# Optimization experiments

Measured on AMD Instinct MI355X. Metric: run time of the kernel, lower is better.

Reference implementation:

```python
import jax, jax.numpy as jnp
import numpy as np

NT, NRV, NR = 100000, 200000, 300000  # tile / road_vertex / road node counts
E = 400000                             # edges per edge type
B, H, P, A = 64, 128, 64, 512          # graphs, hidden, player_state_dim, action_dim


def _gat(h_src, h_dst, src, dst, W, a_s, a_d, b, n_dst):
    # PyG GATConv, heads=1, shared lin for src/dst, no self loops (bipartite)
    hs = h_src @ W                      # [Ns, H]
    hd = h_dst @ W                      # [Nd, H]
    e = jax.nn.leaky_relu((hs @ a_s)[src] + (hd @ a_d)[dst], 0.2)  # [E]
    m = jax.ops.segment_max(e, dst, num_segments=n_dst)
    w = jnp.exp(e - m[dst])
    denom = jax.ops.segment_sum(w, dst, num_segments=n_dst)
    alpha = w / jnp.maximum(denom[dst], 1e-16)                      # segment softmax
    out = jax.ops.segment_sum(alpha[:, None] * hs[src], dst, num_segments=n_dst)
    return out + b


def _mean_pool(x, batch, nb):
    s = jax.ops.segment_sum(x, batch, num_segments=nb)
    c = jax.ops.segment_sum(jnp.ones((x.shape[0],), x.dtype), batch, num_segments=nb)
    return s / jnp.maximum(c, 1.0)[:, None]


def setup_inputs():
    ks = iter(jax.random.split(jax.random.key(0), 64))
    f32 = jnp.float32

    def lin(i, o):
        return (jax.random.normal(next(ks), (i, o), f32) / np.float32(np.sqrt(i)))

    d = {}
    d['x_tile'] = jax.random.normal(next(ks), (NT, 8), f32)
    d['x_rv'] = jax.random.normal(next(ks), (NRV, 13), f32)
    d['x_road'] = jax.random.normal(next(ks), (NR, 4), f32)
    d['x_player'] = jax.random.normal(next(ks), (B, P), f32)
    # node encoders
    d['enc_t_W'] = lin(8, H);  d['enc_t_b'] = jnp.zeros((H,), f32)
    d['enc_rv_W'] = lin(13, H); d['enc_rv_b'] = jnp.zeros((H,), f32)
    d['enc_r_W'] = lin(4, H);  d['enc_r_b'] = jnp.zeros((H,), f32)
    # six GAT convs
    for name in ['rv2t', 't2rv', 'r2rv', 'rv2r', 't2r', 'r2t']:
        d[name + '_W'] = lin(H, H)
        d[name + '_as'] = jax.random.normal(next(ks), (H,), f32) * 0.1
        d[name + '_ad'] = jax.random.normal(next(ks), (H,), f32) * 0.1
        d[name + '_b'] = jnp.zeros((H,), f32)
    # player MLP + output head (input: 3H pooled + H player)
    d['fc1_W'] = lin(P, H); d['fc1_b'] = jnp.zeros((H,), f32)
    d['fc2_W'] = lin(H, H); d['fc2_b'] = jnp.zeros((H,), f32)
    d['out_W'] = lin(4 * H, A); d['out_b'] = jnp.zeros((A,), f32)
    # edges (src bounded by source-type count, dst by dest-type count)
    ri = lambda n, hi: jax.random.randint(n, (E,), 0, hi, jnp.int32)
    d['e_rv2t_src'] = ri(next(ks), NRV); d['e_rv2t_dst'] = ri(next(ks), NT)
    d['e_t2rv_src'] = ri(next(ks), NT);  d['e_t2rv_dst'] = ri(next(ks), NRV)
    d['e_r2rv_src'] = ri(next(ks), NR);  d['e_r2rv_dst'] = ri(next(ks), NRV)
    d['e_rv2r_src'] = ri(next(ks), NRV); d['e_rv2r_dst'] = ri(next(ks), NR)
    d['e_t2r_src'] = ri(next(ks), NT);   d['e_t2r_dst'] = ri(next(ks), NR)
    d['e_r2t_src'] = ri(next(ks), NR);   d['e_r2t_dst'] = ri(next(ks), NT)
    # batch assignment per node type
    d['batch_tile'] = jnp.sort(jax.random.randint(next(ks), (NT,), 0, B, jnp.int32))
    d['batch_rv'] = jnp.sort(jax.random.randint(next(ks), (NRV,), 0, B, jnp.int32))
    d['batch_road'] = jnp.sort(jax.random.randint(next(ks), (NR,), 0, B, jnp.int32))
    return d


def reference(x_tile, x_rv, x_road, x_player,
              enc_t_W, enc_t_b, enc_rv_W, enc_rv_b, enc_r_W, enc_r_b,
              rv2t_W, rv2t_as, rv2t_ad, rv2t_b,
              t2rv_W, t2rv_as, t2rv_ad, t2rv_b,
              r2rv_W, r2rv_as, r2rv_ad, r2rv_b,
              rv2r_W, rv2r_as, rv2r_ad, rv2r_b,
              t2r_W, t2r_as, t2r_ad, t2r_b,
              r2t_W, r2t_as, r2t_ad, r2t_b,
              fc1_W, fc1_b, fc2_W, fc2_b, out_W, out_b,
              e_rv2t_src, e_rv2t_dst, e_t2rv_src, e_t2rv_dst,
              e_r2rv_src, e_r2rv_dst, e_rv2r_src, e_rv2r_dst,
              e_t2r_src, e_t2r_dst, e_r2t_src, e_r2t_dst,
              batch_tile, batch_rv, batch_road):
    # node encoders
    h_t = x_tile @ enc_t_W + enc_t_b
    h_rv = x_rv @ enc_rv_W + enc_rv_b
    h_r = x_road @ enc_r_W + enc_r_b
    # hetero GAT, aggr='sum' over edge types per destination node type
    o_t = (_gat(h_rv, h_t, e_rv2t_src, e_rv2t_dst, rv2t_W, rv2t_as, rv2t_ad, rv2t_b, NT)
           + _gat(h_r, h_t, e_r2t_src, e_r2t_dst, r2t_W, r2t_as, r2t_ad, r2t_b, NT))
    o_rv = (_gat(h_t, h_rv, e_t2rv_src, e_t2rv_dst, t2rv_W, t2rv_as, t2rv_ad, t2rv_b, NRV)
            + _gat(h_r, h_rv, e_r2rv_src, e_r2rv_dst, r2rv_W, r2rv_as, r2rv_ad, r2rv_b, NRV))
    o_r = (_gat(h_rv, h_r, e_rv2r_src, e_rv2r_dst, rv2r_W, rv2r_as, rv2r_ad, rv2r_b, NR)
           + _gat(h_t, h_r, e_t2r_src, e_t2r_dst, t2r_W, t2r_as, t2r_ad, t2r_b, NR))
    # global mean pool per node type, concat -> [B, 3H]
    x_all = jnp.concatenate([_mean_pool(o_t, batch_tile, B),
                             _mean_pool(o_rv, batch_rv, B),
                             _mean_pool(o_r, batch_road, B)], axis=1)
    # player branch
    p = jax.nn.relu(x_player @ fc1_W + fc1_b)
    p = jax.nn.relu(p @ fc2_W + fc2_b)
    x = jnp.concatenate([x_all, p], axis=1)  # [B, 4H]
    return x @ out_W + out_b                 # [B, A]
```

## Files before the change

kernel.cpp:

```cpp
#include <hip/hip_runtime.h>


constexpr int kNT = 100000, kNRV = 200000, kNR = 300000, kE = 400000;
constexpr int kSLOT = 1088;
constexpr int kPSZ  = 6 * kSLOT;
constexpr int kNBE  = 342;
constexpr int kNTH  = kNBE * 256;
constexpr int kEPT  = 5;

constexpr long long OFF_C    = 0;
constexpr long long OFF_VS   = 13056;
constexpr long long OFF_VD   = 13176;
constexpr long long OFF_P4   = 13296;
constexpr long long OFF_LS6  = 39408;
constexpr long long OFF_LD6  = 1239408;
constexpr long long OFF_W16  = 2439408;
constexpr long long OFF_DEN  = 3639408;
constexpr long long OFF_SRV  = 6039408;
constexpr long long OFF_ST   = 7639408;
constexpr long long OFF_SR   = 8039408;

__constant__ const int kDRB[6]  = {0, 100000, 300000, 500000, 800000, 1100000};
__constant__ const int kDLEN[6] = {100000, 200000, 200000, 300000, 300000, 100000};
__constant__ const int kLSB6[6] = {0, 400000, 600000, 200000, 500000, 900000};

__device__ __forceinline__ int lowb(const int* a, int n, int v) {
  int lo = 0, hi = n;
  while (lo < hi) { int mid = (lo + hi) >> 1; if (a[mid] < v) lo = mid + 1; else hi = mid; }
  return lo;
}

static __device__ __forceinline__ unsigned p2h(float a, float b) {
  _Float16 ha = (_Float16)a, hb = (_Float16)b;
  unsigned short ua = __builtin_bit_cast(unsigned short, ha);
  unsigned short ub = __builtin_bit_cast(unsigned short, hb);
  return (unsigned)ua | ((unsigned)ub << 16);
}

__global__ __launch_bounds__(256) void precompute_kernel(
    const float* encW_t, const float* encb_t,
    const float* encW_rv, const float* encb_rv,
    const float* encW_r, const float* encb_r,
    const float* W0, const float* as0, const float* ad0,
    const float* W1, const float* as1, const float* ad1,
    const float* W2, const float* as2, const float* ad2,
    const float* W3, const float* as3, const float* ad3,
    const float* W4, const float* as4, const float* ad4,
    const float* W5, const float* as5, const float* ad5,
    float* Cws, float* vsw, float* vdw, float* P4)
{
  const float* encW[3] = {encW_t, encW_rv, encW_r};
  const float* encb[3] = {encb_t, encb_rv, encb_r};
  const int    Ks[3]   = {8, 13, 4};
  const float* Wv[6]  = {W0, W1, W2, W3, W4, W5};
  const float* asv[6] = {as0, as1, as2, as3, as4, as5};
  const float* adv[6] = {ad0, ad1, ad2, ad3, ad4, ad5};
  const int srcT[6] = {1, 0, 2, 1, 0, 2};
  const int dstT[6] = {0, 1, 1, 2, 2, 0};

  __shared__ float Cl[2176];
  __shared__ float wv[128];

  int et = blockIdx.x;
  int tid = threadIdx.x;
  int st = srcT[et], dt = dstT[et];
  const float* eW = encW[st];
  const float* eB = encb[st];
  int K = Ks[st];
  const float* W = Wv[et];
  const float* a_s = asv[et];
  const float* a_d = adv[et];
  float* Cslot = Cws + et * 2176;

  for (int i = et * 256 + tid; i < 4 * kPSZ; i += 6 * 256) P4[i] = 0.f;

  for (int idx = tid; idx < (K + 1) * 128; idx += 256) {
    int r = idx >> 7, j = idx & 127;
    const float* row = (r < K) ? (eW + r * 128) : eB;
    float acc = 0.f;
    for (int m = 0; m < 128; ++m) acc += row[m] * W[m * 128 + j];
    int o = (r < K) ? (r * 128 + j) : (2048 + j);
    Cl[o] = acc;
    Cslot[o] = acc;
  }
  if (tid < 128) {
    float acc = 0.f;
    for (int j = 0; j < 128; ++j) acc += W[tid * 128 + j] * a_d[j];
    wv[tid] = acc;
  }
  __syncthreads();
  if (tid <= K) {
    const float* row = (tid < K) ? (Cl + tid * 128) : (Cl + 2048);
    float acc = 0.f;
    for (int j = 0; j < 128; ++j) acc += row[j] * a_s[j];
    vsw[et * 20 + (tid < K ? tid : 16)] = acc;
  }
  int KD = Ks[dt];
  if (tid >= 32 && tid <= 32 + KD) {
    int k = tid - 32;
    const float* row = (k < KD) ? (encW[dt] + k * 128) : encb[dt];
    float acc = 0.f;
    for (int m = 0; m < 128; ++m) acc += row[m] * wv[m];
    vdw[et * 20 + (k < KD ? k : 16)] = acc;
  }
}

__global__ __launch_bounds__(256) void prep_kernel(
    const float* __restrict__ x_t, const float* __restrict__ x_rv,
    const float* __restrict__ x_r,
    const int* __restrict__ bt, const int* __restrict__ brv,
    const int* __restrict__ br,
    const float* __restrict__ vsw, const float* __restrict__ vdw,
    uint4* __restrict__ SRVq, uint4* __restrict__ STq, uint2* __restrict__ SRq,
    float* __restrict__ LS6, float* __restrict__ LD6,
    float2* __restrict__ DEN)
{
  int n = blockIdx.x * 256 + threadIdx.x;
  if (n >= kNT + kNRV + kNR) return;
  if (n < kNT) {
    const float* xr = x_t + n * 8;
    float bf = (float)bt[n];
    const float* vsA = vsw + 1 * 20, *vsB = vsw + 4 * 20;
    const float* vdA = vdw + 0 * 20, *vdB = vdw + 5 * 20;
    float x[8]; float a0 = 0, a1 = 0, a2 = 0, a3 = 0;
#pragma unroll
    for (int k = 0; k < 8; ++k) {
      x[k] = xr[k];
      a0 += x[k] * vsA[k]; a1 += x[k] * vsB[k];
      a2 += x[k] * vdA[k]; a3 += x[k] * vdB[k];
    }
    STq[n] = make_uint4(p2h(x[0], x[1]), p2h(x[2], x[3]),
                        p2h(x[4], x[5]), p2h(x[6], x[7]));
    LS6[400000 + n] = a0 + vsA[16];
    LS6[500000 + n] = a1 + vsB[16];
    LD6[n] = a2 + vdA[16];
    LD6[1100000 + n] = a3 + vdB[16];
    DEN[n] = make_float2(0.f, bf);
    DEN[1100000 + n] = make_float2(0.f, bf);
  } else if (n < kNT + kNRV) {
    int m = n - kNT;
    const float* xr = x_rv + m * 13;
    float bf = (float)brv[m];
    const float* vsA = vsw + 0 * 20, *vsB = vsw + 3 * 20;
    const float* vdA = vdw + 1 * 20, *vdB = vdw + 2 * 20;
    float x[13]; float a0 = 0, a1 = 0, a2 = 0, a3 = 0;
#pragma unroll
    for (int k = 0; k < 13; ++k) {
      x[k] = xr[k];
      a0 += x[k] * vsA[k]; a1 += x[k] * vsB[k];
      a2 += x[k] * vdA[k]; a3 += x[k] * vdB[k];
    }
    SRVq[(long long)m * 2] =
        make_uint4(p2h(x[0], x[1]), p2h(x[2], x[3]), p2h(x[4], x[5]), p2h(x[6], x[7]));
    SRVq[(long long)m * 2 + 1] =
        make_uint4(p2h(x[8], x[9]), p2h(x[10], x[11]), p2h(x[12], 0.f), 0);
    LS6[m] = a0 + vsA[16];
    LS6[200000 + m] = a1 + vsB[16];
    LD6[100000 + m] = a2 + vdA[16];
    LD6[300000 + m] = a3 + vdB[16];
    DEN[100000 + m] = make_float2(0.f, bf);
    DEN[300000 + m] = make_float2(0.f, bf);
  } else {
    int m = n - kNT - kNRV;
    const float* xr = x_r + m * 4;
    float bf = (float)br[m];
    const float* vsA = vsw + 2 * 20, *vsB = vsw + 5 * 20;
    const float* vdA = vdw + 3 * 20, *vdB = vdw + 4 * 20;
    float x[4]; float a0 = 0, a1 = 0, a2 = 0, a3 = 0;
#pragma unroll
    for (int k = 0; k < 4; ++k) {
      x[k] = xr[k];
      a0 += x[k] * vsA[k]; a1 += x[k] * vsB[k];
      a2 += x[k] * vdA[k]; a3 += x[k] * vdB[k];
    }
    SRq[m] = make_uint2(p2h(x[0], x[1]), p2h(x[2], x[3]));
    LS6[600000 + m] = a0 + vsA[16];
    LS6[900000 + m] = a1 + vsB[16];
    LD6[500000 + m] = a2 + vdA[16];
    LD6[800000 + m] = a3 + vdB[16];
    DEN[500000 + m] = make_float2(0.f, bf);
    DEN[800000 + m] = make_float2(0.f, bf);
  }
}

__device__ __forceinline__ void pickSD(
    int et,
    const int* s0, const int* s1, const int* s2,
    const int* s3, const int* s4, const int* s5,
    const int* d0, const int* d1, const int* d2,
    const int* d3, const int* d4, const int* d5,
    const int*& sp, const int*& dp)
{
  switch (et) {
    case 0: sp = s0; dp = d0; break;
    case 1: sp = s1; dp = d1; break;
    case 2: sp = s2; dp = d2; break;
    case 3: sp = s3; dp = d3; break;
    case 4: sp = s4; dp = d4; break;
    default: sp = s5; dp = d5; break;
  }
}

__global__ __launch_bounds__(256, 8) void edgeA_kernel(
    const int* s0, const int* s1, const int* s2,
    const int* s3, const int* s4, const int* s5,
    const int* d0, const int* d1, const int* d2,
    const int* d3, const int* d4, const int* d5,
    const float* __restrict__ LS6, const float* __restrict__ LD6,
    _Float16* __restrict__ W16, float* __restrict__ DENf)
{
  int et = blockIdx.x / kNBE;
  int bIdx = blockIdx.x - et * kNBE;
  const int* sp; const int* dp;
  pickSD(et, s0, s1, s2, s3, s4, s5, d0, d1, d2, d3, d4, d5, sp, dp);
  const float* Lsrc = LS6 + kLSB6[et];
  const float* Ldst = LD6 + kDRB[et];
  const int drb = kDRB[et];
  _Float16* Wet = W16 + (long long)et * kE;
  int base = bIdx * 256 + (int)threadIdx.x;

  int s[kEPT], d[kEPT]; bool ok[kEPT];
#pragma unroll
  for (int j = 0; j < kEPT; ++j) {
    int e = base + j * kNTH;
    ok[j] = e < kE;
    int ee = ok[j] ? e : 0;
    s[j] = sp[ee]; d[j] = dp[ee];
  }
  float ls[kEPT];
#pragma unroll
  for (int j = 0; j < kEPT; ++j) ls[j] = Lsrc[s[j]];
  float ld[kEPT];
#pragma unroll
  for (int j = 0; j < kEPT; ++j) ld[j] = Ldst[d[j]];
#pragma unroll
  for (int j = 0; j < kEPT; ++j) {
    float t = ls[j] + ld[j];
    t = t > 0.f ? t : 0.2f * t;
    float w = __expf(t);
    if (ok[j]) {
      Wet[base + j * kNTH] = (_Float16)w;
      unsafeAtomicAdd(&DENf[(long long)(drb + d[j]) * 2], w);
    }
  }
}

template <int TYPE>
__device__ __forceinline__ void ebflow(
    int bIdx,
    const int* __restrict__ sp, const int* __restrict__ dp,
    const uint4* __restrict__ srq4, const uint2* __restrict__ srq2,
    const _Float16* __restrict__ Wet, const float2* __restrict__ DEN2,
    int drb, int dlen, float* lp)
{
  constexpr int K = (TYPE == 0) ? 8 : ((TYPE == 1) ? 13 : 4);
  const int tid = threadIdx.x;
  const int lane = tid & 63;
  int base = bIdx * 256 + tid;

  int s[kEPT], d[kEPT]; bool ok[kEPT];
#pragma unroll
  for (int j = 0; j < kEPT; ++j) {
    int e = base + j * kNTH;
    ok[j] = e < kE;
    int ee = ok[j] ? e : 0;
    s[j] = sp[ee]; d[j] = dp[ee];
  }
  float w[kEPT];
#pragma unroll
  for (int j = 0; j < kEPT; ++j) {
    int e = base + j * kNTH;
    w[j] = (float)Wet[ok[j] ? e : 0];
  }
  uint4 q0[kEPT], q1[kEPT]; uint2 r2v[kEPT];
#pragma unroll
  for (int j = 0; j < kEPT; ++j) {
    if (TYPE == 0) {
      q0[j] = srq4[s[j]];
    } else if (TYPE == 1) {
      q0[j] = srq4[(long long)s[j] * 2];
      q1[j] = srq4[(long long)s[j] * 2 + 1];
    } else {
      r2v[j] = srq2[s[j]];
    }
  }
  float2 f2[kEPT];
#pragma unroll
  for (int j = 0; j < kEPT; ++j) f2[j] = DEN2[drb + d[j]];

#pragma unroll
  for (int j = 0; j < kEPT; ++j) {
    if (!ok[j]) continue;
    int b = (int)f2[j].y;
    float alpha = w[j] / fmaxf(f2[j].x, 1e-16f);
    float xv[K];
    if (TYPE == 0) {
      const _Float16* h = (const _Float16*)&q0[j];
#pragma unroll
      for (int k = 0; k < 8; ++k) xv[k] = (float)h[k];
    } else if (TYPE == 1) {
      const _Float16* h = (const _Float16*)&q0[j];
#pragma unroll
      for (int k = 0; k < 8; ++k) xv[k] = (float)h[k];
      const _Float16* h2 = (const _Float16*)&q1[j];
#pragma unroll
      for (int k = 0; k < 5; ++k) xv[8 + k] = (float)h2[k];
    } else {
      const _Float16* h = (const _Float16*)&r2v[j];
#pragma unroll
      for (int k = 0; k < 4; ++k) xv[k] = (float)h[k];
    }
#pragma unroll
    for (int k = 0; k < K; ++k) atomicAdd(lp + k * 64 + b, alpha * xv[k]);
  }

  for (int base2 = bIdx * 256 + (tid & ~63); base2 < dlen; base2 += kNTH) {
    int j2 = base2 + lane;
    bool a2 = j2 < dlen;
    float2 r2 = a2 ? DEN2[drb + j2] : make_float2(0.f, 0.f);
    int b2 = a2 ? (int)r2.y : (64 + lane);
    int v = (a2 && r2.x > 0.f) ? 1 : 0;
#pragma unroll
    for (int d2 = 1; d2 < 64; d2 <<= 1) {
      int ob = __shfl_up(b2, d2);
      int ov = __shfl_up(v, d2);
      if (lane >= d2 && ob == b2) v += ov;
    }
    int bn = __shfl_down(b2, 1);
    if (((lane == 63) || (bn != b2)) && v > 0) atomicAdd(lp + 1024 + b2, (float)v);
  }
}

__global__ __launch_bounds__(256, 4) void edgeB_kernel(
    const int* s0, const int* s1, const int* s2,
    const int* s3, const int* s4, const int* s5,
    const int* d0, const int* d1, const int* d2,
    const int* d3, const int* d4, const int* d5,
    const uint4* SRVq, const uint4* STq, const uint2* SRq,
    const _Float16* __restrict__ W16, const float2* __restrict__ DEN2,
    float* __restrict__ P4)
{
  __shared__ float lp[kSLOT];
  for (int j = threadIdx.x; j < kSLOT; j += 256) lp[j] = 0.f;
  __syncthreads();
  int et = blockIdx.x / kNBE;
  int bIdx = blockIdx.x - et * kNBE;
  const _Float16* Wet = W16 + (long long)et * kE;
  constexpr int KK[6] = {13, 8, 4, 13, 8, 4};
  switch (et) {
    case 0: ebflow<1>(bIdx, s0, d0, SRVq, nullptr, Wet, DEN2, 0,       100000, lp); break;
    case 1: ebflow<0>(bIdx, s1, d1, STq,  nullptr, Wet, DEN2, 100000,  200000, lp); break;
    case 2: ebflow<2>(bIdx, s2, d2, nullptr, SRq,  Wet, DEN2, 300000,  200000, lp); break;
    case 3: ebflow<1>(bIdx, s3, d3, SRVq, nullptr, Wet, DEN2, 500000,  300000, lp); break;
    case 4: ebflow<0>(bIdx, s4, d4, STq,  nullptr, Wet, DEN2, 800000,  300000, lp); break;
    default: ebflow<2>(bIdx, s5, d5, nullptr, SRq, Wet, DEN2, 1100000, 100000, lp); break;
  }
  __syncthreads();
  int K = KK[et];
  float* slab = P4 + (long long)(blockIdx.x & 3) * kPSZ + (long long)et * kSLOT;
  for (int i = threadIdx.x; i < kSLOT; i += 256) {
    if (i >= K * 64 && i < 1024) continue;
    float v = lp[i];
    if (v != 0.f) unsafeAtomicAdd(&slab[i], v);
  }
}

__global__ __launch_bounds__(128) void tail_kernel(
    const int* __restrict__ bt, const int* __restrict__ brv, const int* __restrict__ br,
    const float* __restrict__ xp,
    const float* __restrict__ fc1W, const float* __restrict__ fc1b,
    const float* __restrict__ fc2W, const float* __restrict__ fc2b,
    const float* __restrict__ outW, const float* __restrict__ outb,
    const float* __restrict__ b_rv2t, const float* __restrict__ b_r2t,
    const float* __restrict__ b_t2rv, const float* __restrict__ b_r2rv,
    const float* __restrict__ b_rv2r, const float* __restrict__ b_t2r,
    const float* __restrict__ Cws, const float* __restrict__ P4,
    float* __restrict__ out)
{
  int b = blockIdx.x >> 3;
  int half = blockIdx.x & 7;
  int tid = threadIdx.x;
  __shared__ float xrow[512];
  __shared__ float p1s[128];
  __shared__ float xps[64];
  __shared__ float psA[15], psB[15];
  __shared__ float part[128];
  __shared__ int cnts[3];

  if (tid < 64) xps[tid] = xp[b * 64 + tid];
  if (tid >= 64 && tid < 67) {
    int t = tid - 64;
    const int* ba = (t == 0) ? bt : (t == 1 ? brv : br);
    int N = (t == 0) ? kNT : (t == 1 ? kNRV : kNR);
    cnts[t] = lowb(ba, N, b + 1) - lowb(ba, N, b);
  }
  __syncthreads();

  float a = fc1b[tid];
  for (int k = 0; k < 64; ++k) a += xps[k] * fc1W[k * 128 + tid];
  p1s[tid] = fmaxf(a, 0.f);
  __syncthreads();
  float a2 = fc2b[tid];
  for (int k = 0; k < 128; ++k) a2 += p1s[k] * fc2W[k * 128 + tid];
  xrow[384 + tid] = fmaxf(a2, 0.f);

  const int etA[3] = {0, 1, 3}, etB[3] = {5, 2, 4};
  const int KAv[3] = {13, 8, 13}, KBv[3] = {4, 4, 8};
  for (int t3 = 0; t3 < 3; ++t3) {
    __syncthreads();
    int eA = etA[t3], eB = etB[t3];
    if (tid < 15) {
      int idx = (tid < 14) ? (tid * 64 + b) : (1024 + b);
      float sum = 0.f;
#pragma unroll
      for (int c = 0; c < 4; ++c) sum += P4[c * kPSZ + eA * kSLOT + idx];
      psA[tid] = sum;
    } else if (tid < 30) {
      int t = tid - 15;
      int idx = (t < 14) ? (t * 64 + b) : (1024 + b);
      float sum = 0.f;
#pragma unroll
      for (int c = 0; c < 4; ++c) sum += P4[c * kPSZ + eB * kSLOT + idx];
      psB[t] = sum;
    }
    __syncthreads();
    int KA = KAv[t3], KB = KBv[t3];
    const float* CA = Cws + eA * 2176;
    const float* CB = Cws + eB * 2176;
    float v = psA[14] * CA[2048 + tid] + psB[14] * CB[2048 + tid];
    for (int k = 0; k < KA; ++k) v += psA[k] * CA[k * 128 + tid];
    for (int k = 0; k < KB; ++k) v += psB[k] * CB[k * 128 + tid];
    float cnt = (float)max(cnts[t3], 1);
    const float* bb1 = (t3 == 0) ? b_rv2t : (t3 == 1 ? b_t2rv : b_rv2r);
    const float* bb2 = (t3 == 0) ? b_r2t  : (t3 == 1 ? b_r2rv : b_t2r);
    xrow[t3 * 128 + tid] = v / cnt + bb1[tid] + bb2[tid];
  }
  __syncthreads();

  {
    int c = half * 64 + (tid & 63);
    int kh = tid >> 6;
    const float* Wc = outW + c;
    float acc = 0.f;
    int k0 = kh * 256;
#pragma unroll 8
    for (int k = k0; k < k0 + 256; ++k) acc += xrow[k] * Wc[(long long)k * 512];
    part[tid] = acc;
    __syncthreads();
    if (tid < 64) out[b * 512 + c] = outb[c] + part[tid] + part[tid + 64];
  }
}

extern "C" void kernel_launch(void* const* d_in, const int* in_sizes, int n_in,
                              void* d_out, int out_size, void* d_ws, size_t ws_size,
                              hipStream_t stream) {
  const float* x_tile   = (const float*)d_in[0];
  const float* x_rv     = (const float*)d_in[1];
  const float* x_road   = (const float*)d_in[2];
  const float* x_player = (const float*)d_in[3];
  const float* enc_t_W  = (const float*)d_in[4];
  const float* enc_t_b  = (const float*)d_in[5];
  const float* enc_rv_W = (const float*)d_in[6];
  const float* enc_rv_b = (const float*)d_in[7];
  const float* enc_r_W  = (const float*)d_in[8];
  const float* enc_r_b  = (const float*)d_in[9];
  const float* W[6]; const float* As[6]; const float* Ad[6]; const float* Bb[6];
  for (int et = 0; et < 6; ++et) {
    W[et]  = (const float*)d_in[10 + 4 * et];
    As[et] = (const float*)d_in[11 + 4 * et];
    Ad[et] = (const float*)d_in[12 + 4 * et];
    Bb[et] = (const float*)d_in[13 + 4 * et];
  }
  const float* fc1W = (const float*)d_in[34];
  const float* fc1b = (const float*)d_in[35];
  const float* fc2W = (const float*)d_in[36];
  const float* fc2b = (const float*)d_in[37];
  const float* outW = (const float*)d_in[38];
  const float* outb = (const float*)d_in[39];
  const int* esrc[6]; const int* edst[6];
  for (int et = 0; et < 6; ++et) {
    esrc[et] = (const int*)d_in[40 + 2 * et];
    edst[et] = (const int*)d_in[41 + 2 * et];
  }
  const int* batch_t  = (const int*)d_in[52];
  const int* batch_rv = (const int*)d_in[53];
  const int* batch_r  = (const int*)d_in[54];

  float* wsF = (float*)d_ws;
  float* Cws  = wsF + OFF_C;
  float* vsw  = wsF + OFF_VS;
  float* vdw  = wsF + OFF_VD;
  float* P4   = wsF + OFF_P4;
  float* LS6  = wsF + OFF_LS6;
  float* LD6  = wsF + OFF_LD6;
  _Float16* W16 = (_Float16*)(wsF + OFF_W16);
  float* DENf = wsF + OFF_DEN;
  float2* DEN2 = (float2*)(wsF + OFF_DEN);
  uint4* SRVq = (uint4*)(wsF + OFF_SRV);
  uint4* STq  = (uint4*)(wsF + OFF_ST);
  uint2* SRq  = (uint2*)(wsF + OFF_SR);
  float* out  = (float*)d_out;

  precompute_kernel<<<6, 256, 0, stream>>>(
      enc_t_W, enc_t_b, enc_rv_W, enc_rv_b, enc_r_W, enc_r_b,
      W[0], As[0], Ad[0], W[1], As[1], Ad[1], W[2], As[2], Ad[2],
      W[3], As[3], Ad[3], W[4], As[4], Ad[4], W[5], As[5], Ad[5],
      Cws, vsw, vdw, P4);

  prep_kernel<<<(kNT + kNRV + kNR + 255) / 256, 256, 0, stream>>>(
      x_tile, x_rv, x_road, batch_t, batch_rv, batch_r, vsw, vdw,
      SRVq, STq, SRq, LS6, LD6, DEN2);

  edgeA_kernel<<<6 * kNBE, 256, 0, stream>>>(
      esrc[0], esrc[1], esrc[2], esrc[3], esrc[4], esrc[5],
      edst[0], edst[1], edst[2], edst[3], edst[4], edst[5],
      LS6, LD6, W16, DENf);

  edgeB_kernel<<<6 * kNBE, 256, 0, stream>>>(
      esrc[0], esrc[1], esrc[2], esrc[3], esrc[4], esrc[5],
      edst[0], edst[1], edst[2], edst[3], edst[4], edst[5],
      SRVq, STq, SRq, W16, DEN2, P4);

  tail_kernel<<<64 * 8, 128, 0, stream>>>(
      batch_t, batch_rv, batch_r, x_player,
      fc1W, fc1b, fc2W, fc2b, outW, outb,
      Bb[0], Bb[5], Bb[1], Bb[2], Bb[3], Bb[4],
      Cws, P4, out);

  (void)in_sizes; (void)n_in; (void)out_size; (void)ws_size;
}
```

Before: 502.6 us.

## Fuse weight precompute and node prep into one kernel with redundant per-block projections

Merges the small precompute kernel and the per-node prep kernel into a single launch. Six blocks compute the composite encoder×W matrices and zero the pool accumulators. The remaining 587 blocks each recompute the attention projection vectors (W·a_s, W·a_d folded through the encoders) in shared memory and then grid-stride over all nodes. This removes one launch and the serial dependency between the two kernels. The cost is redundant per-block matrix-vector work: 128 threads each loop over 6×128 weights before any node is processed.

```diff
diff --git a/kernel.cpp b/kernel.cpp
--- a/kernel.cpp
+++ b/kernel.cpp
@@ -2,15 +2,15 @@
 
 
 constexpr int kNT = 100000, kNRV = 200000, kNR = 300000, kE = 400000;
+constexpr int kNN = kNT + kNRV + kNR;
 constexpr int kSLOT = 1088;
 constexpr int kPSZ  = 6 * kSLOT;
 constexpr int kNBE  = 342;
 constexpr int kNTH  = kNBE * 256;
 constexpr int kEPT  = 5;
+constexpr int kPNB  = 587;
 
 constexpr long long OFF_C    = 0;
-constexpr long long OFF_VS   = 13056;
-constexpr long long OFF_VD   = 13176;
 constexpr long long OFF_P4   = 13296;
 constexpr long long OFF_LS6  = 39408;
 constexpr long long OFF_LD6  = 1239408;
@@ -37,7 +37,11 @@
   return (unsigned)ua | ((unsigned)ub << 16);
 }
 
-__global__ __launch_bounds__(256) void precompute_kernel(
+__global__ __launch_bounds__(256) void prepF_kernel(
+    const float* __restrict__ x_t, const float* __restrict__ x_rv,
+    const float* __restrict__ x_r,
+    const int* __restrict__ bt, const int* __restrict__ brv,
+    const int* __restrict__ br,
     const float* encW_t, const float* encb_t,
     const float* encW_rv, const float* encb_rv,
     const float* encW_r, const float* encb_r,
@@ -47,7 +51,10 @@
     const float* W3, const float* as3, const float* ad3,
     const float* W4, const float* as4, const float* ad4,
     const float* W5, const float* as5, const float* ad5,
-    float* Cws, float* vsw, float* vdw, float* P4)
+    uint4* __restrict__ SRVq, uint4* __restrict__ STq, uint2* __restrict__ SRq,
+    float* __restrict__ LS6, float* __restrict__ LD6,
+    float2* __restrict__ DEN,
+    float* __restrict__ Cws, float* __restrict__ P4)
 {
   const float* encW[3] = {encW_t, encW_rv, encW_r};
   const float* encb[3] = {encb_t, encb_rv, encb_r};
@@ -57,129 +64,129 @@
   const float* adv[6] = {ad0, ad1, ad2, ad3, ad4, ad5};
   const int srcT[6] = {1, 0, 2, 1, 0, 2};
   const int dstT[6] = {0, 1, 1, 2, 2, 0};
-
-  __shared__ float Cl[2176];
-  __shared__ float wv[128];
-
-  int et = blockIdx.x;
   int tid = threadIdx.x;
-  int st = srcT[et], dt = dstT[et];
-  const float* eW = encW[st];
-  const float* eB = encb[st];
-  int K = Ks[st];
-  const float* W = Wv[et];
-  const float* a_s = asv[et];
-  const float* a_d = adv[et];
-  float* Cslot = Cws + et * 2176;
-
-  for (int i = et * 256 + tid; i < 4 * kPSZ; i += 6 * 256) P4[i] = 0.f;
-
-  for (int idx = tid; idx < (K + 1) * 128; idx += 256) {
-    int r = idx >> 7, j = idx & 127;
-    const float* row = (r < K) ? (eW + r * 128) : eB;
-    float acc = 0.f;
-    for (int m = 0; m < 128; ++m) acc += row[m] * W[m * 128 + j];
-    int o = (r < K) ? (r * 128 + j) : (2048 + j);
-    Cl[o] = acc;
-    Cslot[o] = acc;
-  }
+
+  if (blockIdx.x < 6) {
+    int et = blockIdx.x;
+    for (int i = et * 256 + tid; i < 4 * kPSZ; i += 6 * 256) P4[i] = 0.f;
+    int st = srcT[et];
+    int K = Ks[st];
+    const float* eW = encW[st];
+    const float* eB = encb[st];
+    const float* W = Wv[et];
+    float* Cslot = Cws + et * 2176;
+    for (int idx = tid; idx < (K + 1) * 128; idx += 256) {
+      int r = idx >> 7, j = idx & 127;
+      const float* row = (r < K) ? (eW + r * 128) : eB;
+      float acc = 0.f;
+      for (int m = 0; m < 128; ++m) acc += row[m] * W[m * 128 + j];
+      Cslot[(r < K) ? (r * 128 + j) : (2048 + j)] = acc;
+    }
+    return;
+  }
+
+  __shared__ float wsS[6][128], wdS[6][128];
+  __shared__ float vsL[6][20], vdL[6][20];
   if (tid < 128) {
-    float acc = 0.f;
-    for (int j = 0; j < 128; ++j) acc += W[tid * 128 + j] * a_d[j];
-    wv[tid] = acc;
-  }
-  __syncthreads();
-  if (tid <= K) {
-    const float* row = (tid < K) ? (Cl + tid * 128) : (Cl + 2048);
-    float acc = 0.f;
-    for (int j = 0; j < 128; ++j) acc += row[j] * a_s[j];
-    vsw[et * 20 + (tid < K ? tid : 16)] = acc;
-  }
-  int KD = Ks[dt];
-  if (tid >= 32 && tid <= 32 + KD) {
-    int k = tid - 32;
-    const float* row = (k < KD) ? (encW[dt] + k * 128) : encb[dt];
-    float acc = 0.f;
-    for (int m = 0; m < 128; ++m) acc += row[m] * wv[m];
-    vdw[et * 20 + (k < KD ? k : 16)] = acc;
-  }
-}
-
-__global__ __launch_bounds__(256) void prep_kernel(
-    const float* __restrict__ x_t, const float* __restrict__ x_rv,
-    const float* __restrict__ x_r,
-    const int* __restrict__ bt, const int* __restrict__ brv,
-    const int* __restrict__ br,
-    const float* __restrict__ vsw, const float* __restrict__ vdw,
-    uint4* __restrict__ SRVq, uint4* __restrict__ STq, uint2* __restrict__ SRq,
-    float* __restrict__ LS6, float* __restrict__ LD6,
-    float2* __restrict__ DEN)
-{
-  int n = blockIdx.x * 256 + threadIdx.x;
-  if (n >= kNT + kNRV + kNR) return;
-  if (n < kNT) {
-    const float* xr = x_t + n * 8;
-    float bf = (float)bt[n];
-    const float* vsA = vsw + 1 * 20, *vsB = vsw + 4 * 20;
-    const float* vdA = vdw + 0 * 20, *vdB = vdw + 5 * 20;
-    float x[8]; float a0 = 0, a1 = 0, a2 = 0, a3 = 0;
-#pragma unroll
-    for (int k = 0; k < 8; ++k) {
-      x[k] = xr[k];
-      a0 += x[k] * vsA[k]; a1 += x[k] * vsB[k];
-      a2 += x[k] * vdA[k]; a3 += x[k] * vdB[k];
-    }
-    STq[n] = make_uint4(p2h(x[0], x[1]), p2h(x[2], x[3]),
-                        p2h(x[4], x[5]), p2h(x[6], x[7]));
-    LS6[400000 + n] = a0 + vsA[16];
-    LS6[500000 + n] = a1 + vsB[16];
-    LD6[n] = a2 + vdA[16];
-    LD6[1100000 + n] = a3 + vdB[16];
-    DEN[n] = make_float2(0.f, bf);
-    DEN[1100000 + n] = make_float2(0.f, bf);
-  } else if (n < kNT + kNRV) {
-    int m = n - kNT;
-    const float* xr = x_rv + m * 13;
-    float bf = (float)brv[m];
-    const float* vsA = vsw + 0 * 20, *vsB = vsw + 3 * 20;
-    const float* vdA = vdw + 1 * 20, *vdB = vdw + 2 * 20;
-    float x[13]; float a0 = 0, a1 = 0, a2 = 0, a3 = 0;
-#pragma unroll
-    for (int k = 0; k < 13; ++k) {
-      x[k] = xr[k];
-      a0 += x[k] * vsA[k]; a1 += x[k] * vsB[k];
-      a2 += x[k] * vdA[k]; a3 += x[k] * vdB[k];
-    }
-    SRVq[(long long)m * 2] =
-        make_uint4(p2h(x[0], x[1]), p2h(x[2], x[3]), p2h(x[4], x[5]), p2h(x[6], x[7]));
-    SRVq[(long long)m * 2 + 1] =
-        make_uint4(p2h(x[8], x[9]), p2h(x[10], x[11]), p2h(x[12], 0.f), 0);
-    LS6[m] = a0 + vsA[16];
-    LS6[200000 + m] = a1 + vsB[16];
-    LD6[100000 + m] = a2 + vdA[16];
-    LD6[300000 + m] = a3 + vdB[16];
-    DEN[100000 + m] = make_float2(0.f, bf);
-    DEN[300000 + m] = make_float2(0.f, bf);
-  } else {
-    int m = n - kNT - kNRV;
-    const float* xr = x_r + m * 4;
-    float bf = (float)br[m];
-    const float* vsA = vsw + 2 * 20, *vsB = vsw + 5 * 20;
-    const float* vdA = vdw + 3 * 20, *vdB = vdw + 4 * 20;
-    float x[4]; float a0 = 0, a1 = 0, a2 = 0, a3 = 0;
-#pragma unroll
-    for (int k = 0; k < 4; ++k) {
-      x[k] = xr[k];
-      a0 += x[k] * vsA[k]; a1 += x[k] * vsB[k];
-      a2 += x[k] * vdA[k]; a3 += x[k] * vdB[k];
-    }
-    SRq[m] = make_uint2(p2h(x[0], x[1]), p2h(x[2], x[3]));
-    LS6[600000 + m] = a0 + vsA[16];
-    LS6[900000 + m] = a1 + vsB[16];
-    LD6[500000 + m] = a2 + vdA[16];
-    LD6[800000 + m] = a3 + vdB[16];
-    DEN[500000 + m] = make_float2(0.f, bf);
-    DEN[800000 + m] = make_float2(0.f, bf);
+    for (int et = 0; et < 6; ++et) {
+      const float* row = Wv[et] + tid * 128;
+      const float* aS = asv[et];
+      const float* aD = adv[et];
+      float accS = 0.f, accD = 0.f;
+      for (int j = 0; j < 128; ++j) {
+        float w = row[j];
+        accS += w * aS[j];
+        accD += w * aD[j];
+      }
+      wsS[et][tid] = accS;
+      wdS[et][tid] = accD;
+    }
+  }
+  __syncthreads();
+  if (tid < 192) {
+    int et = tid >> 5, k = tid & 31;
+    int st = srcT[et], K = Ks[st];
+    if (k <= K) {
+      const float* row = (k < K) ? (encW[st] + k * 128) : encb[st];
+      float acc = 0.f;
+      for (int m = 0; m < 128; ++m) acc += row[m] * wsS[et][m];
+      vsL[et][k < K ? k : 16] = acc;
+    }
+    int dt = dstT[et], KD = Ks[dt];
+    if (k <= KD) {
+      const float* row = (k < KD) ? (encW[dt] + k * 128) : encb[dt];
+      float acc = 0.f;
+      for (int m = 0; m < 128; ++m) acc += row[m] * wdS[et][m];
+      vdL[et][k < KD ? k : 16] = acc;
+    }
+  }
+  __syncthreads();
+
+  for (int n = (blockIdx.x - 6) * 256 + tid; n < kNN; n += kPNB * 256) {
+    if (n < kNT) {
+      const float* xr = x_t + n * 8;
+      float bf = (float)bt[n];
+      const float* vsA = &vsL[1][0], *vsB = &vsL[4][0];
+      const float* vdA = &vdL[0][0], *vdB = &vdL[5][0];
+      float x[8]; float a0 = 0, a1 = 0, a2 = 0, a3 = 0;
+#pragma unroll
+      for (int k = 0; k < 8; ++k) {
+        x[k] = xr[k];
+        a0 += x[k] * vsA[k]; a1 += x[k] * vsB[k];
+        a2 += x[k] * vdA[k]; a3 += x[k] * vdB[k];
+      }
+      STq[n] = make_uint4(p2h(x[0], x[1]), p2h(x[2], x[3]),
+                          p2h(x[4], x[5]), p2h(x[6], x[7]));
+      LS6[400000 + n] = a0 + vsA[16];
+      LS6[500000 + n] = a1 + vsB[16];
+      LD6[n] = a2 + vdA[16];
+      LD6[1100000 + n] = a3 + vdB[16];
+      DEN[n] = make_float2(0.f, bf);
+      DEN[1100000 + n] = make_float2(0.f, bf);
+    } else if (n < kNT + kNRV) {
+      int m = n - kNT;
+      const float* xr = x_rv + m * 13;
+      float bf = (float)brv[m];
+      const float* vsA = &vsL[0][0], *vsB = &vsL[3][0];
+      const float* vdA = &vdL[1][0], *vdB = &vdL[2][0];
+      float x[13]; float a0 = 0, a1 = 0, a2 = 0, a3 = 0;
+#pragma unroll
+      for (int k = 0; k < 13; ++k) {
+        x[k] = xr[k];
+        a0 += x[k] * vsA[k]; a1 += x[k] * vsB[k];
+        a2 += x[k] * vdA[k]; a3 += x[k] * vdB[k];
+      }
+      SRVq[(long long)m * 2] =
+          make_uint4(p2h(x[0], x[1]), p2h(x[2], x[3]), p2h(x[4], x[5]), p2h(x[6], x[7]));
+      SRVq[(long long)m * 2 + 1] =
+          make_uint4(p2h(x[8], x[9]), p2h(x[10], x[11]), p2h(x[12], 0.f), 0);
+      LS6[m] = a0 + vsA[16];
+      LS6[200000 + m] = a1 + vsB[16];
+      LD6[100000 + m] = a2 + vdA[16];
+      LD6[300000 + m] = a3 + vdB[16];
+      DEN[100000 + m] = make_float2(0.f, bf);
+      DEN[300000 + m] = make_float2(0.f, bf);
+    } else {
+      int m = n - kNT - kNRV;
+      const float* xr = x_r + m * 4;
+      float bf = (float)br[m];
+      const float* vsA = &vsL[2][0], *vsB = &vsL[5][0];
+      const float* vdA = &vdL[3][0], *vdB = &vdL[4][0];
+      float x[4]; float a0 = 0, a1 = 0, a2 = 0, a3 = 0;
+#pragma unroll
+      for (int k = 0; k < 4; ++k) {
+        x[k] = xr[k];
+        a0 += x[k] * vsA[k]; a1 += x[k] * vsB[k];
+        a2 += x[k] * vdA[k]; a3 += x[k] * vdB[k];
+      }
+      SRq[m] = make_uint2(p2h(x[0], x[1]), p2h(x[2], x[3]));
+      LS6[600000 + m] = a0 + vsA[16];
+      LS6[900000 + m] = a1 + vsB[16];
+      LD6[500000 + m] = a2 + vdA[16];
+      LD6[800000 + m] = a3 + vdB[16];
+      DEN[500000 + m] = make_float2(0.f, bf);
+      DEN[800000 + m] = make_float2(0.f, bf);
+    }
   }
 }
 
@@ -488,8 +495,6 @@
 
   float* wsF = (float*)d_ws;
   float* Cws  = wsF + OFF_C;
-  float* vsw  = wsF + OFF_VS;
-  float* vdw  = wsF + OFF_VD;
   float* P4   = wsF + OFF_P4;
   float* LS6  = wsF + OFF_LS6;
   float* LD6  = wsF + OFF_LD6;
@@ -501,15 +506,12 @@
   uint2* SRq  = (uint2*)(wsF + OFF_SR);
   float* out  = (float*)d_out;
 
-  precompute_kernel<<<6, 256, 0, stream>>>(
+  prepF_kernel<<<6 + kPNB, 256, 0, stream>>>(
+      x_tile, x_rv, x_road, batch_t, batch_rv, batch_r,
       enc_t_W, enc_t_b, enc_rv_W, enc_rv_b, enc_r_W, enc_r_b,
       W[0], As[0], Ad[0], W[1], As[1], Ad[1], W[2], As[2], Ad[2],
       W[3], As[3], Ad[3], W[4], As[4], Ad[4], W[5], As[5], Ad[5],
-      Cws, vsw, vdw, P4);
-
-  prep_kernel<<<(kNT + kNRV + kNR + 255) / 256, 256, 0, stream>>>(
-      x_tile, x_rv, x_road, batch_t, batch_rv, batch_r, vsw, vdw,
-      SRVq, STq, SRq, LS6, LD6, DEN2);
+      SRVq, STq, SRq, LS6, LD6, DEN2, Cws, P4);
 
   edgeA_kernel<<<6 * kNBE, 256, 0, stream>>>(
       esrc[0], esrc[1], esrc[2], esrc[3], esrc[4], esrc[5],
```

Result: slower. 517.6 us (+3.0%).
